# Kernel optimization log

Measured on AMD Instinct MI355X. Metric: run time of the kernel, lower is better.

Reference implementation:

```python
import jax, jax.numpy as jnp
import numpy as np

HIDDEN = 1024
NUM_HEADS = 16
HEAD_DIM = HIDDEN // NUM_HEADS
BLOCK_SIZE = 2048
LN_EPS = 1e-12


def layer_norm(x, g, b, eps=LN_EPS):
    mu = jnp.mean(x, axis=-1, keepdims=True)
    var = jnp.mean(jnp.square(x - mu), axis=-1, keepdims=True)
    return (x - mu) * jax.lax.rsqrt(var + eps) * g + b


def setup_inputs() -> dict:
    key = jax.random.key(0)
    ks = jax.random.split(key, 10)
    B, S_CTX, S_Q = 4, 8192, 2048
    scale = 1.0 / np.sqrt(HIDDEN)
    inp = {
        "input_ids": jax.random.normal(ks[0], (B, S_CTX, HIDDEN), jnp.float32),
        "query_input": jax.random.normal(ks[1], (B, S_Q, HIDDEN), jnp.float32),
        "Wq": jax.random.normal(ks[2], (HIDDEN, HIDDEN), jnp.float32) * scale,
        "bq": jnp.zeros((HIDDEN,), jnp.float32),
        "Wk": jax.random.normal(ks[3], (HIDDEN, HIDDEN), jnp.float32) * scale,
        "bk": jnp.zeros((HIDDEN,), jnp.float32),
        "Wv": jax.random.normal(ks[4], (HIDDEN, HIDDEN), jnp.float32) * scale,
        "bv": jnp.zeros((HIDDEN,), jnp.float32),
        "ln_g": jnp.ones((HIDDEN,), jnp.float32),
        "ln_b": jnp.zeros((HIDDEN,), jnp.float32),
        "host_id": 2,
    }
    return inp


def reference(input_ids, query_input, Wq, bq, Wk, bk, Wv, bv, ln_g, ln_b, host_id):
    B = input_ids.shape[0]
    start = host_id * BLOCK_SIZE  # host_id is a static Python int
    # Phase 1: local context encoding (anchor_key is computed in the original
    # but never used downstream, so it does not affect the output)
    local_block = input_ids[:, start:start + BLOCK_SIZE]          # (B, Skv, H)
    local_h = layer_norm(local_block, ln_g, ln_b)
    k = (local_h @ Wk + bk).reshape(B, BLOCK_SIZE, NUM_HEADS, HEAD_DIM)
    v = (local_h @ Wv + bv).reshape(B, BLOCK_SIZE, NUM_HEADS, HEAD_DIM)
    # Phase 2: query encoding; dropout is identity (p=0 / eval mode)
    Sq = query_input.shape[1]
    q_h = layer_norm(query_input, ln_g, ln_b)
    q = (q_h @ Wq + bq).reshape(B, Sq, NUM_HEADS, HEAD_DIM)
    scores = jnp.einsum("bqhd,bkhd->bhqk", q, k) / np.sqrt(HEAD_DIM)
    probs = jax.nn.softmax(scores, axis=-1)                       # (B, H, Sq, Skv)
    ctx = jnp.einsum("bhqk,bkhd->bqhd", probs, v)
    return ctx.reshape(B, Sq, HIDDEN)
```

## Files before the change

kernel.cpp:

```cpp
#include <hip/hip_runtime.h>

#define B_    4
#define SCTX  8192
#define SQ    2048
#define SK    2048
#define HID   1024
#define NH    16
#define HD    64
#define MQ    (B_*SQ)
#define MK    (B_*SK)

typedef float f32x4  __attribute__((ext_vector_type(4)));
typedef short bf16x8 __attribute__((ext_vector_type(8)));

__device__ __forceinline__ unsigned short f2b(float f) {
    union { float f; unsigned u; } v; v.f = f;
    unsigned r = v.u + 0x7FFFu + ((v.u >> 16) & 1u);
    return (unsigned short)(r >> 16);
}

__device__ __forceinline__ int decode_host_id(const unsigned* p) {
    unsigned w0 = p[0];
    int hid;
    if (w0 > 0u && w0 < 8u) hid = (int)w0;
    else if (w0 == 0u) {
        unsigned w1 = p[1];
        hid = (w1 == 0u) ? 0 : (int)__hiloint2double((int)w1, 0);
    } else hid = (int)__uint_as_float(w0);
    if (hid < 0) hid = 0;
    if (hid > SCTX/SK - 1) hid = SCTX/SK - 1;
    return hid;
}

__device__ __forceinline__ void gload16(const unsigned short* g, unsigned short* l) {
    __builtin_amdgcn_global_load_lds(
        (const __attribute__((address_space(1))) void*)g,
        (__attribute__((address_space(3))) void*)l, 16, 0, 0);
}

__global__ __launch_bounds__(256) void ln_tr_kernel(
        const float* __restrict__ query,
        const float* __restrict__ input_ids,
        const unsigned* __restrict__ host_id,
        const float* __restrict__ g,
        const float* __restrict__ lb,
        unsigned short* __restrict__ hq,
        unsigned short* __restrict__ hk,
        const float* __restrict__ Wq,
        const float* __restrict__ Wk,
        const float* __restrict__ Wv,
        unsigned short* __restrict__ Wtq,
        unsigned short* __restrict__ Wtk,
        unsigned short* __restrict__ Wtv) {
    __shared__ unsigned short tile[64][66];
    int bid = blockIdx.x;
    if (bid < 4096) {
        int lane = threadIdx.x & 63;
        int w = threadIdx.x >> 6;
        int row = bid * 4 + w;
        int start = decode_host_id(host_id) * SK;
        const float* src;
        unsigned short* dst;
        if (row < MQ) {
            src = query + (size_t)row * HID;
            dst = hq + (size_t)row * HID;
        } else {
            int r = row - MQ;
            int b = r >> 11, s = r & 2047;
            src = input_ids + ((size_t)b * SCTX + start + s) * HID;
            dst = hk + (size_t)r * HID;
        }
        float4 x[4];
        #pragma unroll
        for (int i = 0; i < 4; i++) x[i] = ((const float4*)src)[lane + i*64];
        float s1 = 0.0f, s2 = 0.0f;
        #pragma unroll
        for (int i = 0; i < 4; i++) {
            s1 += x[i].x + x[i].y + x[i].z + x[i].w;
            s2 += x[i].x*x[i].x + x[i].y*x[i].y + x[i].z*x[i].z + x[i].w*x[i].w;
        }
        #pragma unroll
        for (int off = 1; off < 64; off <<= 1) {
            s1 += __shfl_xor(s1, off, 64);
            s2 += __shfl_xor(s2, off, 64);
        }
        float mu   = s1 * (1.0f / HID);
        float var  = s2 * (1.0f / HID) - mu * mu;
        float rstd = rsqrtf(fmaxf(var, 0.0f) + 1e-12f);
        #pragma unroll
        for (int i = 0; i < 4; i++) {
            float4 gv = ((const float4*)g)[lane + i*64];
            float4 bv = ((const float4*)lb)[lane + i*64];
            ushort4 o;
            o.x = f2b((x[i].x - mu) * rstd * gv.x + bv.x);
            o.y = f2b((x[i].y - mu) * rstd * gv.y + bv.y);
            o.z = f2b((x[i].z - mu) * rstd * gv.z + bv.z);
            o.w = f2b((x[i].w - mu) * rstd * gv.w + bv.w);
            ((ushort4*)dst)[lane + i*64] = o;
        }
    } else {
        int id = bid - 4096;
        int z = id >> 8;
        int tid = id & 255;
        const float* src = (z == 0) ? Wq : (z == 1) ? Wk : Wv;
        unsigned short* dst = (z == 0) ? Wtq : (z == 1) ? Wtk : Wtv;
        int tx = threadIdx.x & 63;
        int ty = threadIdx.x >> 6;
        int k0 = (tid & 15) * 64;
        int n0 = (tid >> 4) * 64;
        for (int i = ty; i < 64; i += 4)
            tile[i][tx] = f2b(src[(size_t)(k0 + i) * HID + n0 + tx]);
        __syncthreads();
        for (int i = ty; i < 64; i += 4)
            dst[(size_t)(n0 + i) * HID + k0 + tx] = tile[tx][i];
    }
}

#define BM 128
#define BN 128
#define BKg 32

__global__ __launch_bounds__(256, 3) void gemm3_kernel(
        const unsigned short* __restrict__ hq,
        const unsigned short* __restrict__ hk,
        const unsigned short* __restrict__ Wtq,
        const unsigned short* __restrict__ Wtk,
        const unsigned short* __restrict__ Wtv,
        const float* __restrict__ bq,
        const float* __restrict__ bk,
        const float* __restrict__ bv,
        unsigned short* __restrict__ Qb,
        unsigned short* __restrict__ Kb,
        unsigned short* __restrict__ Vtb) {
    __shared__ __align__(16) unsigned short As[2][BM * BKg];
    __shared__ __align__(16) unsigned short Bs[2][BN * BKg];

    int z = blockIdx.z;
    const unsigned short* A  = (z == 0) ? hq : hk;
    const unsigned short* Bt = (z == 0) ? Wtq : (z == 1) ? Wtk : Wtv;
    const float* bias        = (z == 0) ? bq  : (z == 1) ? bk  : bv;
    unsigned short* out      = (z == 0) ? Qb  : (z == 1) ? Kb  : Vtb;
    float scale = (z == 0) ? 0.18033688f : 1.0f;
    int epi = (z == 2);

    int t = threadIdx.x;
    int lane = t & 63;
    int w = t >> 6;
    int wr = w >> 1, wc = w & 1;
    int qd = lane >> 4, c = lane & 15;

    int bid = (int)(blockIdx.y * gridDim.x + blockIdx.x);
    int xcd = bid & 7, kk = bid >> 3;
    int bx = xcd * 8 + (kk & 7);
    int by = kk >> 3;
    size_t m0 = (size_t)bx * BM;
    size_t n0 = (size_t)by * BN;

    int s0 = t, s1 = t + 256;
    int ar0 = s0 >> 2, ac0 = (s0 & 3) * 8;
    int ar1 = s1 >> 2, ac1 = (s1 & 3) * 8;

#define STAGE(buf, kk0) do { \
    gload16(A  + (m0 + ar0) * HID + (kk0) + ac0, &As[buf][s0 * 8]); \
    gload16(A  + (m0 + ar1) * HID + (kk0) + ac1, &As[buf][s1 * 8]); \
    gload16(Bt + (n0 + ar0) * HID + (kk0) + ac0, &Bs[buf][s0 * 8]); \
    gload16(Bt + (n0 + ar1) * HID + (kk0) + ac1, &Bs[buf][s1 * 8]); \
} while (0)

#define COMPUTE(buf) do { \
    bf16x8 a[4], b[4]; \
    _Pragma("unroll") \
    for (int mi = 0; mi < 4; mi++) \
        a[mi] = *(const bf16x8*)(&As[buf][(wr*64 + mi*16 + c) * BKg + qd*8]); \
    _Pragma("unroll") \
    for (int ni = 0; ni < 4; ni++) \
        b[ni] = *(const bf16x8*)(&Bs[buf][(wc*64 + ni*16 + c) * BKg + qd*8]); \
    _Pragma("unroll") \
    for (int mi = 0; mi < 4; mi++) \
        _Pragma("unroll") \
        for (int ni = 0; ni < 4; ni++) \
            acc[mi][ni] = __builtin_amdgcn_mfma_f32_16x16x32_bf16(a[mi], b[ni], acc[mi][ni], 0, 0, 0); \
} while (0)

    f32x4 acc[4][4] = {};
    STAGE(0, 0);
    int cur = 0;
    for (int kt = 0; kt < HID/BKg - 1; kt++) {
        STAGE(cur ^ 1, (kt + 1) * BKg);
        asm volatile("s_waitcnt vmcnt(4)" ::: "memory");
        __builtin_amdgcn_s_barrier();
        COMPUTE(cur);
        asm volatile("s_waitcnt lgkmcnt(0)" ::: "memory");
        __builtin_amdgcn_s_barrier();
        cur ^= 1;
    }
    asm volatile("s_waitcnt vmcnt(0)" ::: "memory");
    __builtin_amdgcn_s_barrier();
    COMPUTE(cur);
#undef STAGE
#undef COMPUTE

    #pragma unroll
    for (int ni = 0; ni < 4; ni++) {
        int n = (int)n0 + wc*64 + ni*16 + c;
        float bn = bias[n];
        #pragma unroll
        for (int mi = 0; mi < 4; mi++) {
            int mbase = (int)m0 + wr*64 + mi*16 + qd*4;
            if (epi == 0) {
                #pragma unroll
                for (int r = 0; r < 4; r++)
                    out[(size_t)(mbase + r) * HID + n] = f2b((acc[mi][ni][r] + bn) * scale);
            } else {
                int bb = mbase >> 11, s = mbase & 2047;
                int h = n >> 6, d = n & 63;
                ushort4 pk;
                pk.x = f2b(acc[mi][ni][0] + bn);
                pk.y = f2b(acc[mi][ni][1] + bn);
                pk.z = f2b(acc[mi][ni][2] + bn);
                pk.w = f2b(acc[mi][ni][3] + bn);
                *(ushort4*)(out + (((size_t)(bb*NH + h))*HD + d)*SK + s) = pk;
            }
        }
    }
}

__global__ __launch_bounds__(64) void attn_kernel(
        const unsigned short* __restrict__ Q,
        const unsigned short* __restrict__ K,
        const unsigned short* __restrict__ Vt,
        float* __restrict__ out) {
    __shared__ __align__(16) unsigned short P[64][72];
    int lane = threadIdx.x;
    int qd = lane >> 4, c = lane & 15;
    int q0 = blockIdx.x * 64;
    int h  = blockIdx.y;
    int b  = blockIdx.z;

    bf16x8 qf[4][2];
    #pragma unroll
    for (int mi = 0; mi < 4; mi++)
        #pragma unroll
        for (int ks = 0; ks < 2; ks++)
            qf[mi][ks] = *(const bf16x8*)(Q + ((size_t)(b*SQ + q0 + mi*16 + c))*HID + h*HD + ks*32 + qd*8);

    float lsum[4][4];
    f32x4 o[4][4] = {};
    #pragma unroll
    for (int mi = 0; mi < 4; mi++)
        #pragma unroll
        for (int r = 0; r < 4; r++) lsum[mi][r] = 0.0f;

    for (int kt = 0; kt < SK/64; kt++) {
        int key0 = kt * 64;
        bf16x8 kf[4][2];
        #pragma unroll
        for (int ni = 0; ni < 4; ni++)
            #pragma unroll
            for (int ks = 0; ks < 2; ks++)
                kf[ni][ks] = *(const bf16x8*)(K + ((size_t)(b*SK + key0 + ni*16 + c))*HID + h*HD + ks*32 + qd*8);
        f32x4 s[4][4] = {};
        #pragma unroll
        for (int mi = 0; mi < 4; mi++)
            #pragma unroll
            for (int ni = 0; ni < 4; ni++) {
                s[mi][ni] = __builtin_amdgcn_mfma_f32_16x16x32_bf16(qf[mi][0], kf[ni][0], s[mi][ni], 0, 0, 0);
                s[mi][ni] = __builtin_amdgcn_mfma_f32_16x16x32_bf16(qf[mi][1], kf[ni][1], s[mi][ni], 0, 0, 0);
            }
        bf16x8 vf[4][2];
        #pragma unroll
        for (int ni = 0; ni < 4; ni++)
            #pragma unroll
            for (int ks = 0; ks < 2; ks++)
                vf[ni][ks] = *(const bf16x8*)(Vt + (((size_t)(b*NH + h))*HD + ni*16 + c)*SK + key0 + ks*32 + qd*8);
        #pragma unroll
        for (int mi = 0; mi < 4; mi++) {
            #pragma unroll
            for (int ni = 0; ni < 4; ni++)
                #pragma unroll
                for (int r = 0; r < 4; r++) {
                    float p = __builtin_amdgcn_exp2f(fminf(s[mi][ni][r], 50.0f));
                    s[mi][ni][r] = p;
                    lsum[mi][r] += p;
                }
            #pragma unroll
            for (int ni = 0; ni < 4; ni++)
                #pragma unroll
                for (int r = 0; r < 4; r++)
                    P[mi*16 + qd*4 + r][ni*16 + c] = f2b(s[mi][ni][r]);
        }
        asm volatile("s_waitcnt lgkmcnt(0)" ::: "memory");
        bf16x8 pf[4][2];
        #pragma unroll
        for (int mi = 0; mi < 4; mi++)
            #pragma unroll
            for (int ks = 0; ks < 2; ks++)
                pf[mi][ks] = *(const bf16x8*)(&P[mi*16 + c][ks*32 + qd*8]);
        #pragma unroll
        for (int mi = 0; mi < 4; mi++)
            #pragma unroll
            for (int ni = 0; ni < 4; ni++) {
                o[mi][ni] = __builtin_amdgcn_mfma_f32_16x16x32_bf16(pf[mi][0], vf[ni][0], o[mi][ni], 0, 0, 0);
                o[mi][ni] = __builtin_amdgcn_mfma_f32_16x16x32_bf16(pf[mi][1], vf[ni][1], o[mi][ni], 0, 0, 0);
            }
    }
    #pragma unroll
    for (int mi = 0; mi < 4; mi++)
        #pragma unroll
        for (int r = 0; r < 4; r++) {
            float l = lsum[mi][r];
            for (int off = 1; off < 16; off <<= 1) l += __shfl_xor(l, off, 16);
            lsum[mi][r] = 1.0f / l;
        }
    #pragma unroll
    for (int mi = 0; mi < 4; mi++)
        #pragma unroll
        for (int ni = 0; ni < 4; ni++)
            #pragma unroll
            for (int r = 0; r < 4; r++) {
                int m = q0 + mi*16 + qd*4 + r;
                out[((size_t)(b*SQ + m))*HID + h*HD + ni*16 + c] = o[mi][ni][r] * lsum[mi][r];
            }
}

extern "C" void kernel_launch(void* const* d_in, const int* in_sizes, int n_in,
                              void* d_out, int out_size, void* d_ws, size_t ws_size,
                              hipStream_t stream) {
    const float *input_ids = nullptr, *query = nullptr;
    const float *Ws[3] = {nullptr, nullptr, nullptr};
    const float *bs[5] = {nullptr, nullptr, nullptr, nullptr, nullptr};
    const unsigned *hostid = nullptr;
    int wi = 0, bi = 0;
    for (int i = 0; i < n_in; i++) {
        long sz = in_sizes[i];
        if      (sz == 33554432) input_ids = (const float*)d_in[i];
        else if (sz == 8388608)  query     = (const float*)d_in[i];
        else if (sz == 1048576)  { if (wi < 3) Ws[wi++] = (const float*)d_in[i]; }
        else if (sz == 1024)     { if (bi < 5) bs[bi++] = (const float*)d_in[i]; }
        else if (sz == 1 || sz == 2) hostid = (const unsigned*)d_in[i];
    }
    if (n_in != 11 || !input_ids || !query || wi != 3 || bi != 5 || !hostid) {
        input_ids = (const float*)d_in[0];  query = (const float*)d_in[1];
        Ws[0] = (const float*)d_in[2]; bs[0] = (const float*)d_in[3];
        Ws[1] = (const float*)d_in[4]; bs[1] = (const float*)d_in[5];
        Ws[2] = (const float*)d_in[6]; bs[2] = (const float*)d_in[7];
        bs[3] = (const float*)d_in[8]; bs[4] = (const float*)d_in[9];
        hostid = (const unsigned*)d_in[10];
    }
    const float *Wq = Ws[0], *Wk = Ws[1], *Wv = Ws[2];
    const float *bq = bs[0], *bk = bs[1], *bv = bs[2], *ln_g = bs[3], *ln_b = bs[4];
    float* out = (float*)d_out;

    char* ws = (char*)d_ws;
    unsigned short* hq  = (unsigned short*)ws; ws += (size_t)MQ * HID * 2;
    unsigned short* hk  = (unsigned short*)ws; ws += (size_t)MK * HID * 2;
    unsigned short* Wtq = (unsigned short*)ws; ws += (size_t)HID * HID * 2;
    unsigned short* Wtk = (unsigned short*)ws; ws += (size_t)HID * HID * 2;
    unsigned short* Wtv = (unsigned short*)ws; ws += (size_t)HID * HID * 2;
    unsigned short* Qb  = (unsigned short*)ws; ws += (size_t)MQ * HID * 2;
    unsigned short* Kb  = (unsigned short*)ws; ws += (size_t)MK * HID * 2;
    unsigned short* Vtb = (unsigned short*)ws; ws += (size_t)MK * HID * 2;

    ln_tr_kernel<<<4096 + 768, 256, 0, stream>>>(
        query, input_ids, hostid, ln_g, ln_b, hq, hk,
        Wq, Wk, Wv, Wtq, Wtk, Wtv);
    gemm3_kernel<<<dim3(MQ/BM, HID/BN, 3), 256, 0, stream>>>(
        hq, hk, Wtq, Wtk, Wtv, bq, bk, bv, Qb, Kb, Vtb);
    attn_kernel<<<dim3(SQ/64, NH, B_), 64, 0, stream>>>(Qb, Kb, Vtb, out);
}
```

Baseline: 418.2 us.

## Split attention key range across two waves and remap blocks for L2 locality

Each attention block now runs two wavefronts that each process half of the key tiles for the same 64 queries. The partial outputs and row sums are combined through shared memory before normalization and the store. The block index is remapped so that blocks sharing a (batch, head) panel are grouped per XCD-like stride of 8, which should improve K/V cache reuse. This doubles the wave-level parallelism per query tile, at the cost of an extra reduction through LDS and two barriers.

```diff
diff --git a/kernel.cpp b/kernel.cpp
--- a/kernel.cpp
+++ b/kernel.cpp
@@ -225,17 +225,24 @@
     }
 }
 
-__global__ __launch_bounds__(64) void attn_kernel(
+__global__ __launch_bounds__(128) void attn_kernel(
         const unsigned short* __restrict__ Q,
         const unsigned short* __restrict__ K,
         const unsigned short* __restrict__ Vt,
         float* __restrict__ out) {
-    __shared__ __align__(16) unsigned short P[64][72];
-    int lane = threadIdx.x;
+    __shared__ __align__(16) unsigned short P[2][64][72];
+    __shared__ float lsumsh[64];
+    int t = threadIdx.x;
+    int w = t >> 6;
+    int lane = t & 63;
     int qd = lane >> 4, c = lane & 15;
-    int q0 = blockIdx.x * 64;
-    int h  = blockIdx.y;
-    int b  = blockIdx.z;
+    int bid = blockIdx.x;
+    int x = bid & 7, local = bid >> 3;
+    int panel = x * 8 + (local >> 5);
+    int qt = local & 31;
+    int h = panel & 15;
+    int b = panel >> 4;
+    int q0 = qt * 64;
 
     bf16x8 qf[4][2];
     #pragma unroll
@@ -251,7 +258,7 @@
         #pragma unroll
         for (int r = 0; r < 4; r++) lsum[mi][r] = 0.0f;
 
-    for (int kt = 0; kt < SK/64; kt++) {
+    for (int kt = w * (SK/128); kt < (w + 1) * (SK/128); kt++) {
         int key0 = kt * 64;
         bf16x8 kf[4][2];
         #pragma unroll
@@ -287,7 +294,7 @@
             for (int ni = 0; ni < 4; ni++)
                 #pragma unroll
                 for (int r = 0; r < 4; r++)
-                    P[mi*16 + qd*4 + r][ni*16 + c] = f2b(s[mi][ni][r]);
+                    P[w][mi*16 + qd*4 + r][ni*16 + c] = f2b(s[mi][ni][r]);
         }
         asm volatile("s_waitcnt lgkmcnt(0)" ::: "memory");
         bf16x8 pf[4][2];
@@ -295,7 +302,7 @@
         for (int mi = 0; mi < 4; mi++)
             #pragma unroll
             for (int ks = 0; ks < 2; ks++)
-                pf[mi][ks] = *(const bf16x8*)(&P[mi*16 + c][ks*32 + qd*8]);
+                pf[mi][ks] = *(const bf16x8*)(&P[w][mi*16 + c][ks*32 + qd*8]);
         #pragma unroll
         for (int mi = 0; mi < 4; mi++)
             #pragma unroll
@@ -310,17 +317,43 @@
         for (int r = 0; r < 4; r++) {
             float l = lsum[mi][r];
             for (int off = 1; off < 16; off <<= 1) l += __shfl_xor(l, off, 16);
-            lsum[mi][r] = 1.0f / l;
-        }
-    #pragma unroll
-    for (int mi = 0; mi < 4; mi++)
-        #pragma unroll
-        for (int ni = 0; ni < 4; ni++)
-            #pragma unroll
-            for (int r = 0; r < 4; r++) {
-                int m = q0 + mi*16 + qd*4 + r;
-                out[((size_t)(b*SQ + m))*HID + h*HD + ni*16 + c] = o[mi][ni][r] * lsum[mi][r];
+            lsum[mi][r] = l;
+        }
+    __syncthreads();
+    float* oshare = (float*)&P[0][0][0];
+    if (w == 1) {
+        #pragma unroll
+        for (int mi = 0; mi < 4; mi++)
+            #pragma unroll
+            for (int ni = 0; ni < 4; ni++)
+                *(f32x4*)&oshare[((mi*4 + ni)*64 + lane)*4] = o[mi][ni];
+        if (c == 0) {
+            #pragma unroll
+            for (int mi = 0; mi < 4; mi++)
+                #pragma unroll
+                for (int r = 0; r < 4; r++)
+                    lsumsh[mi*16 + qd*4 + r] = lsum[mi][r];
+        }
+    }
+    __syncthreads();
+    if (w == 0) {
+        #pragma unroll
+        for (int mi = 0; mi < 4; mi++) {
+            float inv[4];
+            #pragma unroll
+            for (int r = 0; r < 4; r++)
+                inv[r] = 1.0f / (lsum[mi][r] + lsumsh[mi*16 + qd*4 + r]);
+            #pragma unroll
+            for (int ni = 0; ni < 4; ni++) {
+                f32x4 o1 = *(const f32x4*)&oshare[((mi*4 + ni)*64 + lane)*4];
+                #pragma unroll
+                for (int r = 0; r < 4; r++) {
+                    int m = q0 + mi*16 + qd*4 + r;
+                    out[((size_t)(b*SQ + m))*HID + h*HD + ni*16 + c] = (o[mi][ni][r] + o1[r]) * inv[r];
+                }
             }
+        }
+    }
 }
 
 extern "C" void kernel_launch(void* const* d_in, const int* in_sizes, int n_in,
@@ -366,5 +399,5 @@
         Wq, Wk, Wv, Wtq, Wtk, Wtv);
     gemm3_kernel<<<dim3(MQ/BM, HID/BN, 3), 256, 0, stream>>>(
         hq, hk, Wtq, Wtk, Wtv, bq, bk, bv, Qb, Kb, Vtb);
-    attn_kernel<<<dim3(SQ/64, NH, B_), 64, 0, stream>>>(Qb, Kb, Vtb, out);
-}
+    attn_kernel<<<2048, 128, 0, stream>>>(Qb, Kb, Vtb, out);
+}
```

New measurement: 451.5 us. 7.9% more time.
